# Performance work log

Measured on AMD Instinct MI355X. Metric: run time of the kernel, lower is better.

Reference implementation:

```python
import jax, jax.numpy as jnp
import numpy as np

HEADS = 8


def setup_inputs() -> dict:
    key = jax.random.key(0)
    k1, k2, k3, k4, k5 = jax.random.split(key, 5)
    bt, b_sz, n, dim = 2, 4, 1024, 512
    inner6 = 3072  # inner_dim * 6 where inner_dim = heads * dim_head = 512
    return {
        "x": jax.random.normal(k1, (bt, b_sz, n, dim), dtype=jnp.float32),
        "W_qkv": jax.random.normal(k2, (dim, inner6), dtype=jnp.float32) * 0.02,
        "b_qkv": jax.random.normal(k3, (inner6,), dtype=jnp.float32) * 0.02,
        "W_out": jax.random.normal(k4, (1024, dim), dtype=jnp.float32) * 0.02,
        "b_out": jax.random.normal(k5, (dim,), dtype=jnp.float32) * 0.02,
    }


def reference(x, W_qkv, b_qkv, W_out, b_out):
    bt, b_sz, n, dim = x.shape
    # to_qkv: Linear(dim, 3072) -> reshape (bt,b,n,3,H,hd) -> transpose(2,4)
    qkv = (x @ W_qkv + b_qkv).reshape(bt, b_sz, n, 3, HEADS, -1)
    qkv = qkv.transpose(0, 1, 4, 3, 2, 5)  # (bt, b, H, 3, n, hd)
    q, k, v = qkv[:, :, :, 0], qkv[:, :, :, 1], qkv[:, :, :, 2]
    scale = (dim // HEADS) ** -0.5  # faithful: uses dim//heads, not per-head width
    attn = jax.nn.softmax(jnp.einsum("abhnd,abhmd->abhnm", q * scale, k), axis=-1)
    out = jnp.einsum("abhnm,abhmd->abhnd", attn, v)
    out = out.transpose(0, 1, 3, 2, 4).reshape(bt, b_sz, n, -1)  # (bt,b,n,H*hd)
    return out @ W_out + b_out
```

## Files before the change

kernel.cpp:

```cpp
#include <hip/hip_runtime.h>

typedef __attribute__((ext_vector_type(4))) float f32x4;
typedef __attribute__((ext_vector_type(16))) float f32x16;
typedef __attribute__((ext_vector_type(8))) __bf16 bf16x8;
typedef __attribute__((ext_vector_type(8))) unsigned short ushortx8;
typedef __attribute__((ext_vector_type(4))) unsigned short ushortx4;
typedef unsigned short u16;
typedef unsigned int u32;

#define AS1 __attribute__((address_space(1)))
#define AS3 __attribute__((address_space(3)))

__device__ __forceinline__ void gld_lds16(const void* g, void* s) {
  __builtin_amdgcn_global_load_lds((AS1 void*)g, (AS3 void*)s, 16, 0, 0);
}

__device__ __forceinline__ u16 f2bf(float f) {
  unsigned int u = __float_as_uint(f);
  unsigned int r = (u + 0x7FFFu + ((u >> 16) & 1u)) >> 16;
  return (u16)r;
}

#define QSCALE 0.1803368801111244f

__global__ __launch_bounds__(256) void prep_fused(
    const float* __restrict__ x, u16* __restrict__ xb,
    const float* __restrict__ bqkv, float* __restrict__ bq2,
    const float* __restrict__ Wqkv, u16* __restrict__ wqkvt,
    const float* __restrict__ Wout, u16* __restrict__ woutt) {
  const int gid = blockIdx.x, tid = threadIdx.x;
  if (gid < 2048) {
    const int i = (gid * 256 + tid) * 8;
    const float4 a = *(const float4*)&x[i];
    const float4 b = *(const float4*)&x[i + 4];
    ushortx8 o;
    o[0] = f2bf(a.x); o[1] = f2bf(a.y); o[2] = f2bf(a.z); o[3] = f2bf(a.w);
    o[4] = f2bf(b.x); o[5] = f2bf(b.y); o[6] = f2bf(b.z); o[7] = f2bf(b.w);
    *(ushortx8*)&xb[i] = o;
    return;
  }
  __shared__ float tile[32][33];
  const int tx = tid & 31, ty = tid >> 5;
  if (gid < 3584) {
    const int t = gid - 2048;
    const int c0 = (t % 96) * 32, r0 = (t / 96) * 32;
    #pragma unroll
    for (int i = ty; i < 32; i += 8)
      tile[i][tx] = Wqkv[(size_t)(r0 + i) * 3072 + c0 + tx];
    __syncthreads();
    #pragma unroll
    for (int i = ty; i < 32; i += 8) {
      const float sc = (c0 + i < 1024) ? QSCALE : 1.0f;
      wqkvt[(size_t)(c0 + i) * 512 + r0 + tx] = f2bf(tile[tx][i] * sc);
    }
    return;
  }
  if (gid < 4096) {
    const int t = gid - 3584;
    const int c0 = (t % 16) * 32, r0 = (t / 16) * 32;
    #pragma unroll
    for (int i = ty; i < 32; i += 8)
      tile[i][tx] = Wout[(size_t)(r0 + i) * 512 + c0 + tx];
    __syncthreads();
    #pragma unroll
    for (int i = ty; i < 32; i += 8)
      woutt[(size_t)(c0 + i) * 1024 + r0 + tx] = f2bf(tile[tx][i]);
    return;
  }
  const int i = (gid - 4096) * 256 + tid;
  if (i < 3072) bq2[i] = bqkv[i] * (i < 1024 ? QSCALE : 1.0f);
}

template <int BM, int BN, int BK, int OUT_BF16>
__global__ __launch_bounds__(256, 4) void gemm_bt(const u16* __restrict__ A,
                                                  const u16* __restrict__ Bt,
                                                  const float* __restrict__ bias,
                                                  void* __restrict__ Cv,
                                                  int M, int N, int K) {
  constexpr int RPC = 512 / BK;
  constexpr int LPR = BK / 8;
  constexpr int MASK = LPR - 1;
  constexpr int P = 64 / BK > 0 ? 64 / BK : 1;
  constexpr int CA = BM / RPC, CB = BN / RPC;
  constexpr int CAW = CA / 4, CBW = CB / 4;
  constexpr int VM = CAW + CBW;
  constexpr int FM = BM / 32, FN = BN / 32;
  constexpr int KS = BK / 32;

  __shared__ __attribute__((aligned(16))) u16 As[2][BM * BK];
  __shared__ __attribute__((aligned(16))) u16 Bs[2][BN * BK];
  const int nwg = gridDim.x * gridDim.y;
  int bid = blockIdx.y * gridDim.x + blockIdx.x;
  if ((nwg & 7) == 0) bid = (bid & 7) * (nwg >> 3) + (bid >> 3);
  const int n0 = (bid % gridDim.x) * BN, m0 = (bid / gridDim.x) * BM;
  const int tid = threadIdx.x;
  const int w = tid >> 6, l = tid & 63;
  const int wr = w >> 1, wc = w & 1;
  const int lr = l >> 4, lc = l & 15;
  f32x4 acc[FM][FN] = {};

#define GSTAGE(bi, k0)                                                          \
  do {                                                                          \
    _Pragma("unroll") for (int i = 0; i < CAW; ++i) {                           \
      const int c = w * CAW + i;                                                \
      const int row = c * RPC + l / LPR;                                        \
      const int col = ((l % LPR) ^ ((row / P) & MASK)) * 8;                     \
      gld_lds16(&A[(size_t)(m0 + row) * K + (k0) + col], &As[bi][c * 512]);     \
    }                                                                           \
    _Pragma("unroll") for (int i = 0; i < CBW; ++i) {                           \
      const int c = w * CBW + i;                                                \
      const int row = c * RPC + l / LPR;                                        \
      const int col = ((l % LPR) ^ ((row / P) & MASK)) * 8;                     \
      gld_lds16(&Bt[(size_t)(n0 + row) * K + (k0) + col], &Bs[bi][c * 512]);    \
    }                                                                           \
  } while (0)

#define GCOMP(bi)                                                                      \
  do {                                                                                 \
    _Pragma("unroll") for (int ks = 0; ks < KS; ++ks) {                                \
      bf16x8 af[FM], bfr[FN];                                                          \
      _Pragma("unroll") for (int m = 0; m < FM; ++m) {                                 \
        const int row = wr * (BM / 2) + m * 16 + lc;                                   \
        af[m] = *(const bf16x8*)&As[bi][row * BK +                                     \
                                        (((ks * 4 + lr) ^ ((row / P) & MASK)) << 3)];  \
      }                                                                                \
      _Pragma("unroll") for (int n = 0; n < FN; ++n) {                                 \
        const int row = wc * (BN / 2) + n * 16 + lc;                                   \
        bfr[n] = *(const bf16x8*)&Bs[bi][row * BK +                                    \
                                         (((ks * 4 + lr) ^ ((row / P) & MASK)) << 3)]; \
      }                                                                                \
      __builtin_amdgcn_s_setprio(1);                                                   \
      _Pragma("unroll") for (int m = 0; m < FM; ++m)                                   \
          _Pragma("unroll") for (int n = 0; n < FN; ++n)                               \
              acc[m][n] =                                                              \
          __builtin_amdgcn_mfma_f32_16x16x32_bf16(af[m], bfr[n], acc[m][n], 0, 0, 0);  \
      __builtin_amdgcn_s_setprio(0);                                                   \
    }                                                                                  \
  } while (0)

  GSTAGE(0, 0);
  int buf = 0;
  for (int k0 = BK; k0 < K; k0 += BK) {
    GSTAGE(buf ^ 1, k0);
    if constexpr (VM == 2)
      asm volatile("s_waitcnt vmcnt(2)" ::: "memory");
    else if constexpr (VM == 3)
      asm volatile("s_waitcnt vmcnt(3)" ::: "memory");
    else if constexpr (VM == 4)
      asm volatile("s_waitcnt vmcnt(4)" ::: "memory");
    else
      asm volatile("s_waitcnt vmcnt(8)" ::: "memory");
    __builtin_amdgcn_s_barrier();
    __builtin_amdgcn_sched_barrier(0);
    GCOMP(buf);
    __builtin_amdgcn_s_barrier();
    buf ^= 1;
  }
  asm volatile("s_waitcnt vmcnt(0)" ::: "memory");
  __builtin_amdgcn_s_barrier();
  __builtin_amdgcn_sched_barrier(0);
  GCOMP(buf);
#undef GSTAGE
#undef GCOMP

  #pragma unroll
  for (int n = 0; n < FN; ++n) {
    const int col = n0 + wc * (BN / 2) + n * 16 + lc;
    const float bv = bias[col];
    #pragma unroll
    for (int m = 0; m < FM; ++m) {
      #pragma unroll
      for (int r = 0; r < 4; ++r) {
        const int row = m0 + wr * (BM / 2) + m * 16 + lr * 4 + r;
        const float v = acc[m][n][r] + bv;
        if (OUT_BF16)
          ((u16*)Cv)[(size_t)row * N + col] = f2bf(v);
        else
          ((float*)Cv)[(size_t)row * N + col] = v;
      }
    }
  }
}

__global__ __launch_bounds__(512, 2) void gemm_qkv_8ph(const u16* __restrict__ A,
                                                       const u16* __restrict__ Bt,
                                                       const float* __restrict__ bias,
                                                       u16* __restrict__ C,
                                                       u16* __restrict__ vt,
                                                       int M, int N, int K) {
  __shared__ __attribute__((aligned(16))) u16 SMEM[57344];
  u16* const AsP[2] = {SMEM, SMEM + 16384};
  u16* const BsP[2] = {SMEM + 32768, SMEM + 45056};
  const int nwg = gridDim.x;
  int bid = blockIdx.x;
  if ((nwg & 7) == 0) bid = (bid & 7) * (nwg >> 3) + (bid >> 3);
  const int ntile = N / 192;
  const int n0 = (bid % ntile) * 192, m0 = (bid / ntile) * 256;
  const int tid = threadIdx.x;
  const int w = tid >> 6, l = tid & 63;
  const int wr = w >> 2, wc = w & 3;
  const int lr = l >> 4, lc = l & 15;
  f32x4 acc[8][3] = {};
  bf16x8 af[2][2], bfv[3][2];

#define STAGE_A(bi, kt, h)                                                          \
  do {                                                                              \
    _Pragma("unroll") for (int cc = 0; cc < 2; ++cc) {                              \
      const int cib = (h) * 1024 + (cc * 8 + w) * 64;                               \
      const int ci = cib + l;                                                       \
      const int row = ci >> 3, ck = ci & 7;                                         \
      gld_lds16(&A[(size_t)(m0 + row) * K + (kt) * 64 + ((ck ^ (row & 7)) << 3)],   \
                &AsP[bi][cib * 8]);                                                 \
    }                                                                               \
  } while (0)

#define STAGE_B(bi, kt, t)                                                          \
  do {                                                                              \
    const int cib = (t) * 512 + w * 64;                                             \
    const int ci = cib + l;                                                         \
    const int row = ci >> 3, ck = ci & 7;                                           \
    gld_lds16(&Bt[(size_t)(n0 + row) * K + (kt) * 64 + ((ck ^ (row & 7)) << 3)],    \
              &BsP[bi][cib * 8]);                                                   \
  } while (0)

#define RD_A(bi, mp)                                                                \
  do {                                                                              \
    _Pragma("unroll") for (int m2 = 0; m2 < 2; ++m2)                                \
      _Pragma("unroll") for (int ks = 0; ks < 2; ++ks) {                            \
        const int row = wr * 128 + (2 * (mp) + m2) * 16 + lc;                       \
        af[m2][ks] = *(const bf16x8*)&AsP[bi][row * 64 +                            \
                                              (((ks * 4 + lr) ^ (lc & 7)) << 3)];   \
      }                                                                             \
  } while (0)

#define RD_B(bi)                                                                    \
  do {                                                                              \
    _Pragma("unroll") for (int n = 0; n < 3; ++n)                                   \
      _Pragma("unroll") for (int ks = 0; ks < 2; ++ks) {                            \
        const int row = wc * 48 + n * 16 + lc;                                      \
        bfv[n][ks] = *(const bf16x8*)&BsP[bi][row * 64 +                            \
                                              (((ks * 4 + lr) ^ (lc & 7)) << 3)];   \
      }                                                                             \
  } while (0)

#define MM(mp)                                                                      \
  do {                                                                              \
    __builtin_amdgcn_s_setprio(1);                                                  \
    _Pragma("unroll") for (int m2 = 0; m2 < 2; ++m2)                                \
      _Pragma("unroll") for (int n = 0; n < 3; ++n)                                 \
        _Pragma("unroll") for (int ks = 0; ks < 2; ++ks)                            \
          acc[2 * (mp) + m2][n] = __builtin_amdgcn_mfma_f32_16x16x32_bf16(          \
              af[m2][ks], bfv[n][ks], acc[2 * (mp) + m2][n], 0, 0, 0);              \
    __builtin_amdgcn_s_setprio(0);                                                  \
  } while (0)

#define BARC()                                                                      \
  do {                                                                              \
    __builtin_amdgcn_s_barrier();                                                   \
    asm volatile("s_waitcnt lgkmcnt(0)" ::: "memory");                              \
    __builtin_amdgcn_sched_barrier(0);                                              \
  } while (0)

  STAGE_B(0, 0, 0); STAGE_B(0, 0, 1); STAGE_B(0, 0, 2);
  STAGE_A(0, 0, 0); STAGE_A(0, 0, 1);
  STAGE_B(1, 1, 0); STAGE_B(1, 1, 1);
  asm volatile("s_waitcnt vmcnt(2)" ::: "memory");
  __builtin_amdgcn_s_barrier();
  __builtin_amdgcn_sched_barrier(0);

  const int NI = K >> 7;
  for (int i = 0; i < NI; ++i) {
    const bool nl = (i < NI - 1);
    const int tO = 2 * i + 1, tE2 = 2 * i + 2, tO2 = 2 * i + 3;
    RD_B(0); RD_A(0, 0);
    STAGE_B(1, tO, 2); STAGE_A(1, tO, 0); STAGE_A(1, tO, 1);
    BARC(); MM(0);
    __builtin_amdgcn_s_barrier();
    RD_A(0, 1);
    if (nl) STAGE_B(0, tE2, 0);
    BARC(); MM(1);
    __builtin_amdgcn_s_barrier();
    RD_A(0, 2);
    if (nl) STAGE_B(0, tE2, 1);
    BARC(); MM(2);
    __builtin_amdgcn_s_barrier();
    RD_A(0, 3);
    if (nl) STAGE_B(0, tE2, 2);
    BARC(); MM(3);
    if (nl) asm volatile("s_waitcnt vmcnt(3)" ::: "memory");
    else    asm volatile("s_waitcnt vmcnt(0)" ::: "memory");
    __builtin_amdgcn_s_barrier();
    __builtin_amdgcn_sched_barrier(0);
    RD_B(1); RD_A(1, 0);
    if (nl) STAGE_A(0, tE2, 0);
    BARC(); MM(0);
    __builtin_amdgcn_s_barrier();
    RD_A(1, 1);
    if (nl) STAGE_A(0, tE2, 1);
    BARC(); MM(1);
    __builtin_amdgcn_s_barrier();
    RD_A(1, 2);
    if (nl) STAGE_B(1, tO2, 0);
    BARC(); MM(2);
    __builtin_amdgcn_s_barrier();
    RD_A(1, 3);
    if (nl) STAGE_B(1, tO2, 1);
    BARC(); MM(3);
    if (nl) {
      asm volatile("s_waitcnt vmcnt(2)" ::: "memory");
      __builtin_amdgcn_s_barrier();
      __builtin_amdgcn_sched_barrier(0);
    }
  }
#undef STAGE_A
#undef STAGE_B
#undef RD_A
#undef RD_B
#undef MM
#undef BARC

  __builtin_amdgcn_s_barrier();
  const int b_idx = m0 >> 10;
  const int tok0 = m0 & 1023;
  #pragma unroll
  for (int n = 0; n < 3; ++n) {
    const int gc = n0 + wc * 48 + n * 16 + lc;
    const float bv = bias[gc];
    if (gc < 2048) {
      #pragma unroll
      for (int m = 0; m < 8; ++m)
        #pragma unroll
        for (int r = 0; r < 4; ++r) {
          const int row = wr * 128 + m * 16 + lr * 4 + r;
          SMEM[row * 192 + wc * 48 + n * 16 + lc] = f2bf(acc[m][n][r] + bv);
        }
    } else {
      const int hd = gc - 2048;
      u16* vrow = vt + ((size_t)(b_idx * 8 + (hd >> 7)) * 128 + (hd & 127)) * 1024;
      #pragma unroll
      for (int m = 0; m < 8; ++m) {
        const int tok = tok0 + wr * 128 + m * 16 + lr * 4;
        ushortx4 o;
        o[0] = f2bf(acc[m][n][0] + bv);
        o[1] = f2bf(acc[m][n][1] + bv);
        o[2] = f2bf(acc[m][n][2] + bv);
        o[3] = f2bf(acc[m][n][3] + bv);
        *(ushortx4*)&vrow[tok] = o;
      }
    }
  }
  __builtin_amdgcn_s_barrier();
  #pragma unroll
  for (int it = 0; it < 12; ++it) {
    const int chunk = it * 512 + tid;
    const int row = chunk / 24, c16 = chunk % 24;
    if (n0 + c16 * 8 < 2048) {
      const bf16x8 v = *(const bf16x8*)&SMEM[row * 192 + c16 * 8];
      *(bf16x8*)&C[(size_t)(m0 + row) * N + n0 + c16 * 8] = v;
    }
  }
}

__global__ __launch_bounds__(256, 2) void attn_fwd(const u16* __restrict__ qkv,
                                                   const u16* __restrict__ vt,
                                                   u16* __restrict__ attn_out) {
  __shared__ __attribute__((aligned(16))) u16 Ks[2][64 * 128];
  __shared__ __attribute__((aligned(16))) u16 Vs[2][64 * 128];
  const int orig = blockIdx.y * 8 + blockIdx.x;
  const int swz = (orig & 7) * 64 + (orig >> 3);
  const int bh = swz >> 3, b = bh >> 3, h = bh & 7;
  const int q0 = (swz & 7) * 128;
  const int tid = threadIdx.x, w = tid >> 6, l = tid & 63;
  const int ll = l & 31, hi = l >> 5;
  const int wq0 = q0 + w * 32;
  const u16* Qb = qkv + (size_t)(b * 1024 + wq0) * 3072 + h * 128;
  const u16* Kb = qkv + (size_t)(b * 1024) * 3072 + 1024 + h * 128;
  const u16* Vb = vt + (size_t)(b * 8 + h) * 128 * 1024;

  bf16x8 bq[8];
  #pragma unroll
  for (int s = 0; s < 8; ++s)
    bq[s] = *(const bf16x8*)&Qb[(size_t)ll * 3072 + s * 16 + hi * 8];
  asm volatile("s_waitcnt vmcnt(0)" ::: "memory");

  bf16x8 ones;
  #pragma unroll
  for (int i = 0; i < 8; ++i) ones[i] = (__bf16)1.0f;

  const u16* sb[8];
  int dst0;
  if (w < 2) {
    #pragma unroll
    for (int j = 0; j < 8; ++j) {
      const int r = w * 32 + j * 4 + (l >> 4);
      const int c = l & 15;
      sb[j] = Kb + (size_t)r * 3072 + ((c ^ (r & 15)) << 3);
    }
    dst0 = w * 4096;
  } else {
    #pragma unroll
    for (int j = 0; j < 8; ++j) {
      const int r2 = (w - 2) * 32 + j * 4 + (l >> 4);
      const int c = l & 15;
      const int d = ((c >> 3) ^ ((r2 >> 3) & 1)) * 64 + (r2 >> 5) * 32 + (r2 & 31);
      const int kc = (c & 7) ^ (r2 & 7);
      sb[j] = Vb + (size_t)d * 1024 + (kc << 3);
    }
    dst0 = (w - 2) * 4096;
  }

#define STAGE(bi, tt)                                                            \
  do {                                                                           \
    if (w < 2) {                                                                 \
      _Pragma("unroll") for (int j = 0; j < 8; ++j)                              \
          gld_lds16(sb[j] + (size_t)(tt)*196608, &Ks[bi][dst0 + j * 512]);       \
    } else {                                                                     \
      _Pragma("unroll") for (int j = 0; j < 8; ++j)                              \
          gld_lds16(sb[j] + (size_t)(tt)*64, &Vs[bi][dst0 + j * 512]);           \
    }                                                                            \
  } while (0)

#define QK(Kt)                                                                     \
  do {                                                                            \
    st0 = (f32x16){};                                                             \
    st1 = (f32x16){};                                                             \
    __builtin_amdgcn_s_setprio(1);                                                \
    _Pragma("unroll") for (int s = 0; s < 8; ++s) {                               \
      const int ch = ((s * 2 + hi) ^ (ll & 15)) << 3;                             \
      const bf16x8 ak0 = *(const bf16x8*)&(Kt)[ll * 128 + ch];                    \
      const bf16x8 ak1 = *(const bf16x8*)&(Kt)[(32 + ll) * 128 + ch];             \
      st0 = __builtin_amdgcn_mfma_f32_32x32x16_bf16(ak0, bq[s], st0, 0, 0, 0);    \
      st1 = __builtin_amdgcn_mfma_f32_32x32x16_bf16(ak1, bq[s], st1, 0, 0, 0);    \
    }                                                                             \
    __builtin_amdgcn_s_setprio(0);                                                \
  } while (0)

#define SOFTMAX()                                                                  \
  do {                                                                            \
    _Pragma("unroll") for (int kb = 0; kb < 2; ++kb) {                            \
      float pe[16];                                                               \
      _Pragma("unroll") for (int r = 0; r < 16; ++r)                              \
          pe[r] = exp2f(kb ? st1[r] : st0[r]);                                    \
      _Pragma("unroll") for (int j = 0; j < 8; ++j) {                             \
        u32 d_;                                                                   \
        asm("v_cvt_pk_bf16_f32 %0, %1, %2"                                        \
            : "=v"(d_)                                                            \
            : "v"(pe[2 * j]), "v"(pe[2 * j + 1]));                                \
        mm[kb * 8 + j] = d_;                                                      \
      }                                                                           \
      asm volatile("v_permlane32_swap_b32 %0, %1"                                 \
                   : "+v"(mm[kb * 8 + 0]), "+v"(mm[kb * 8 + 2]));                 \
      asm volatile("v_permlane32_swap_b32 %0, %1"                                 \
                   : "+v"(mm[kb * 8 + 1]), "+v"(mm[kb * 8 + 3]));                 \
      asm volatile("v_permlane32_swap_b32 %0, %1"                                 \
                   : "+v"(mm[kb * 8 + 4]), "+v"(mm[kb * 8 + 6]));                 \
      asm volatile("v_permlane32_swap_b32 %0, %1"                                 \
                   : "+v"(mm[kb * 8 + 5]), "+v"(mm[kb * 8 + 7]));                 \
    }                                                                             \
  } while (0)

#define PV(Vt_)                                                                    \
  do {                                                                            \
    __builtin_amdgcn_s_setprio(1);                                                \
    _Pragma("unroll") for (int kb = 0; kb < 2; ++kb) {                            \
      _Pragma("unroll") for (int s2 = 0; s2 < 2; ++s2) {                          \
        union { u32 u[4]; bf16x8 v; } pu;                                         \
        pu.u[0] = mm[kb * 8 + s2 * 4 + 0];                                        \
        pu.u[1] = mm[kb * 8 + s2 * 4 + 1];                                        \
        pu.u[2] = mm[kb * 8 + s2 * 4 + 2];                                        \
        pu.u[3] = mm[kb * 8 + s2 * 4 + 3];                                        \
        const bf16x8 pa = pu.v;                                                   \
        acc_l = __builtin_amdgcn_mfma_f32_32x32x16_bf16(pa, ones, acc_l, 0, 0, 0);\
        _Pragma("unroll") for (int db = 0; db < 4; ++db) {                        \
          const int r2 = (db & 1) * 32 + ll;                                      \
          const int c = ((((db >> 1) ^ ((ll >> 3) & 1)) << 3) |                   \
                         ((kb * 4 + s2 * 2 + hi) ^ (ll & 7)));                    \
          const bf16x8 bv = *(const bf16x8*)&(Vt_)[r2 * 128 + c * 8];             \
          acc_o[db] =                                                             \
              __builtin_amdgcn_mfma_f32_32x32x16_bf16(pa, bv, acc_o[db], 0, 0, 0);\
        }                                                                         \
      }                                                                           \
    }                                                                             \
    __builtin_amdgcn_s_setprio(0);                                                \
  } while (0)

  f32x16 acc_o[4] = {};
  f32x16 acc_l = {};
  f32x16 st0, st1;
  u32 mm[16];

  STAGE(0, 0);
  int buf = 0;
  for (int t = 0; t < 15; ++t) {
    STAGE(buf ^ 1, t + 1);
    asm volatile("s_waitcnt vmcnt(8)" ::: "memory");
    __builtin_amdgcn_s_barrier();
    __builtin_amdgcn_sched_barrier(0);
    QK(Ks[buf]);
    SOFTMAX();
    PV(Vs[buf]);
    __builtin_amdgcn_s_barrier();
    buf ^= 1;
  }
  asm volatile("s_waitcnt vmcnt(0)" ::: "memory");
  __builtin_amdgcn_s_barrier();
  __builtin_amdgcn_sched_barrier(0);
  QK(Ks[buf]);
  SOFTMAX();
  PV(Vs[buf]);

#undef STAGE
#undef QK
#undef SOFTMAX
#undef PV

  float inv[16];
  #pragma unroll
  for (int r = 0; r < 16; ++r) inv[r] = __builtin_amdgcn_rcpf(acc_l[r]);
  u16* Ob = attn_out + (size_t)(b * 1024 + wq0) * 1024 + h * 128;
  #pragma unroll
  for (int db = 0; db < 4; ++db)
    #pragma unroll
    for (int r = 0; r < 16; ++r) {
      const int q = (r & 3) + 8 * (r >> 2) + 4 * hi;
      Ob[(size_t)q * 1024 + db * 32 + ll] = f2bf(acc_o[db][r] * inv[r]);
    }
}

extern "C" void kernel_launch(void* const* d_in, const int* in_sizes, int n_in,
                              void* d_out, int out_size, void* d_ws, size_t ws_size,
                              hipStream_t stream) {
  const float* x = (const float*)d_in[0];
  const float* Wqkv = (const float*)d_in[1];
  const float* bqkv = (const float*)d_in[2];
  const float* Wout = (const float*)d_in[3];
  const float* bout = (const float*)d_in[4];
  float* out = (float*)d_out;

  char* ws = (char*)d_ws;
  u16* xb    = (u16*)(ws);
  u16* wqkvt = (u16*)(ws + 8388608);
  u16* woutt = (u16*)(ws + 8388608 + 3145728);
  u16* qkvb  = (u16*)(ws + 12582912);
  u16* vtb   = (u16*)(ws + 62914560);
  u16* aob   = (u16*)(ws + 79691776);
  float* bq2 = (float*)aob;

  prep_fused<<<4108, 256, 0, stream>>>(x, xb, bqkv, bq2, Wqkv, wqkvt, Wout, woutt);

  gemm_qkv_8ph<<<dim3(512), 512, 0, stream>>>(xb, wqkvt, bq2, qkvb, vtb,
                                              8192, 3072, 512);

  attn_fwd<<<dim3(8, 64), 256, 0, stream>>>(qkvb, vtb, aob);

  gemm_bt<128, 64, 32, 0><<<dim3(8, 64), 256, 0, stream>>>(aob, woutt, bout, out,
                                                           8192, 512, 1024);
}
```

Before: 116.7 us.

## Restructure double-buffer loops to use a single barrier per stage

Reworks the double-buffered pipelines in the GEMM, fused QKV GEMM and attention kernels so each iteration waits for all outstanding loads, issues one barrier, then issues the next stage's loads before computing. This drops the trailing barrier per iteration, and in the ping-pong GEMM it moves the LDS wait ahead of the barrier and merges adjacent barrier pairs. The cost is that the next tile's global loads are issued later, after the barrier, and the wait is now vmcnt(0), so less load latency may be hidden behind compute.

```diff
diff --git a/kernel.cpp b/kernel.cpp
--- a/kernel.cpp
+++ b/kernel.cpp
@@ -83,7 +83,6 @@
   constexpr int P = 64 / BK > 0 ? 64 / BK : 1;
   constexpr int CA = BM / RPC, CB = BN / RPC;
   constexpr int CAW = CA / 4, CBW = CB / 4;
-  constexpr int VM = CAW + CBW;
   constexpr int FM = BM / 32, FN = BN / 32;
   constexpr int KS = BK / 32;
 
@@ -140,26 +139,14 @@
 
   GSTAGE(0, 0);
   int buf = 0;
-  for (int k0 = BK; k0 < K; k0 += BK) {
-    GSTAGE(buf ^ 1, k0);
-    if constexpr (VM == 2)
-      asm volatile("s_waitcnt vmcnt(2)" ::: "memory");
-    else if constexpr (VM == 3)
-      asm volatile("s_waitcnt vmcnt(3)" ::: "memory");
-    else if constexpr (VM == 4)
-      asm volatile("s_waitcnt vmcnt(4)" ::: "memory");
-    else
-      asm volatile("s_waitcnt vmcnt(8)" ::: "memory");
+  for (int k0 = 0; k0 < K; k0 += BK) {
+    asm volatile("s_waitcnt vmcnt(0)" ::: "memory");
     __builtin_amdgcn_s_barrier();
     __builtin_amdgcn_sched_barrier(0);
+    if (k0 + BK < K) GSTAGE(buf ^ 1, k0 + BK);
     GCOMP(buf);
-    __builtin_amdgcn_s_barrier();
     buf ^= 1;
   }
-  asm volatile("s_waitcnt vmcnt(0)" ::: "memory");
-  __builtin_amdgcn_s_barrier();
-  __builtin_amdgcn_sched_barrier(0);
-  GCOMP(buf);
 #undef GSTAGE
 #undef GCOMP
 
@@ -254,10 +241,10 @@
     __builtin_amdgcn_s_setprio(0);                                                  \
   } while (0)
 
-#define BARC()                                                                      \
+#define SEAL()                                                                      \
   do {                                                                              \
+    asm volatile("s_waitcnt lgkmcnt(0)" ::: "memory");                              \
     __builtin_amdgcn_s_barrier();                                                   \
-    asm volatile("s_waitcnt lgkmcnt(0)" ::: "memory");                              \
     __builtin_amdgcn_sched_barrier(0);                                              \
   } while (0)
 
@@ -274,50 +261,44 @@
     const int tO = 2 * i + 1, tE2 = 2 * i + 2, tO2 = 2 * i + 3;
     RD_B(0); RD_A(0, 0);
     STAGE_B(1, tO, 2); STAGE_A(1, tO, 0); STAGE_A(1, tO, 1);
-    BARC(); MM(0);
-    __builtin_amdgcn_s_barrier();
+    SEAL(); MM(0);
     RD_A(0, 1);
     if (nl) STAGE_B(0, tE2, 0);
-    BARC(); MM(1);
-    __builtin_amdgcn_s_barrier();
+    SEAL(); MM(1);
     RD_A(0, 2);
     if (nl) STAGE_B(0, tE2, 1);
-    BARC(); MM(2);
-    __builtin_amdgcn_s_barrier();
+    SEAL(); MM(2);
     RD_A(0, 3);
     if (nl) STAGE_B(0, tE2, 2);
-    BARC(); MM(3);
+    asm volatile("s_waitcnt lgkmcnt(0)" ::: "memory");
     if (nl) asm volatile("s_waitcnt vmcnt(3)" ::: "memory");
     else    asm volatile("s_waitcnt vmcnt(0)" ::: "memory");
     __builtin_amdgcn_s_barrier();
     __builtin_amdgcn_sched_barrier(0);
+    MM(3);
     RD_B(1); RD_A(1, 0);
     if (nl) STAGE_A(0, tE2, 0);
-    BARC(); MM(0);
-    __builtin_amdgcn_s_barrier();
+    SEAL(); MM(0);
     RD_A(1, 1);
     if (nl) STAGE_A(0, tE2, 1);
-    BARC(); MM(1);
-    __builtin_amdgcn_s_barrier();
+    SEAL(); MM(1);
     RD_A(1, 2);
     if (nl) STAGE_B(1, tO2, 0);
-    BARC(); MM(2);
-    __builtin_amdgcn_s_barrier();
+    SEAL(); MM(2);
     RD_A(1, 3);
     if (nl) STAGE_B(1, tO2, 1);
-    BARC(); MM(3);
-    if (nl) {
-      asm volatile("s_waitcnt vmcnt(2)" ::: "memory");
-      __builtin_amdgcn_s_barrier();
-      __builtin_amdgcn_sched_barrier(0);
-    }
+    asm volatile("s_waitcnt lgkmcnt(0)" ::: "memory");
+    if (nl) asm volatile("s_waitcnt vmcnt(2)" ::: "memory");
+    __builtin_amdgcn_s_barrier();
+    __builtin_amdgcn_sched_barrier(0);
+    MM(3);
   }
 #undef STAGE_A
 #undef STAGE_B
 #undef RD_A
 #undef RD_B
 #undef MM
-#undef BARC
+#undef SEAL
 
   __builtin_amdgcn_s_barrier();
   const int b_idx = m0 >> 10;
@@ -491,23 +472,16 @@
 
   STAGE(0, 0);
   int buf = 0;
-  for (int t = 0; t < 15; ++t) {
-    STAGE(buf ^ 1, t + 1);
-    asm volatile("s_waitcnt vmcnt(8)" ::: "memory");
+  for (int t = 0; t < 16; ++t) {
+    asm volatile("s_waitcnt vmcnt(0)" ::: "memory");
     __builtin_amdgcn_s_barrier();
     __builtin_amdgcn_sched_barrier(0);
+    if (t < 15) STAGE(buf ^ 1, t + 1);
     QK(Ks[buf]);
     SOFTMAX();
     PV(Vs[buf]);
-    __builtin_amdgcn_s_barrier();
     buf ^= 1;
   }
-  asm volatile("s_waitcnt vmcnt(0)" ::: "memory");
-  __builtin_amdgcn_s_barrier();
-  __builtin_amdgcn_sched_barrier(0);
-  QK(Ks[buf]);
-  SOFTMAX();
-  PV(Vs[buf]);
 
 #undef STAGE
 #undef QK
```

Result: no change. 118.2 us (+1.3%).

## Shrink attention blocks to two waves and drop LDS double buffering

Applied to the files above, without the earlier changes.

The attention kernel now runs 128-thread blocks covering 64 queries each, launching twice as many blocks. K/V staging moves to a single LDS buffer (32KB instead of 64KB), loaded synchronously each tile with vmcnt(0), so more blocks can share a CU. The first QK MFMA uses a zero constant instead of explicit clears, and exp2f is replaced by the hardware exp2 builtin. The trade-off is losing load/compute overlap inside a block and doubling K/V global traffic per query, in the hope that the extra resident blocks hide the latency instead.

```diff
diff --git a/kernel.cpp b/kernel.cpp
--- a/kernel.cpp
+++ b/kernel.cpp
@@ -361,15 +361,15 @@
   }
 }
 
-__global__ __launch_bounds__(256, 2) void attn_fwd(const u16* __restrict__ qkv,
+__global__ __launch_bounds__(128, 4) void attn_fwd(const u16* __restrict__ qkv,
                                                    const u16* __restrict__ vt,
                                                    u16* __restrict__ attn_out) {
-  __shared__ __attribute__((aligned(16))) u16 Ks[2][64 * 128];
-  __shared__ __attribute__((aligned(16))) u16 Vs[2][64 * 128];
-  const int orig = blockIdx.y * 8 + blockIdx.x;
-  const int swz = (orig & 7) * 64 + (orig >> 3);
-  const int bh = swz >> 3, b = bh >> 3, h = bh & 7;
-  const int q0 = (swz & 7) * 128;
+  __shared__ __attribute__((aligned(16))) u16 Ks[64 * 128];
+  __shared__ __attribute__((aligned(16))) u16 Vs[64 * 128];
+  const int orig = blockIdx.y * 16 + blockIdx.x;
+  const int swz = (orig & 7) * 128 + (orig >> 3);
+  const int bh = swz >> 4, b = bh >> 3, h = bh & 7;
+  const int q0 = (swz & 15) * 64;
   const int tid = threadIdx.x, w = tid >> 6, l = tid & 63;
   const int ll = l & 31, hi = l >> 5;
   const int wq0 = q0 + w * 32;
@@ -386,49 +386,52 @@
   bf16x8 ones;
   #pragma unroll
   for (int i = 0; i < 8; ++i) ones[i] = (__bf16)1.0f;
-
-  const u16* sb[8];
-  int dst0;
-  if (w < 2) {
-    #pragma unroll
-    for (int j = 0; j < 8; ++j) {
-      const int r = w * 32 + j * 4 + (l >> 4);
+  const f32x16 fz = {};
+
+  const u16* sb[16];
+  if (w == 0) {
+    #pragma unroll
+    for (int j = 0; j < 16; ++j) {
+      const int r = j * 4 + (l >> 4);
       const int c = l & 15;
       sb[j] = Kb + (size_t)r * 3072 + ((c ^ (r & 15)) << 3);
     }
-    dst0 = w * 4096;
   } else {
     #pragma unroll
-    for (int j = 0; j < 8; ++j) {
-      const int r2 = (w - 2) * 32 + j * 4 + (l >> 4);
+    for (int j = 0; j < 16; ++j) {
+      const int r2 = j * 4 + (l >> 4);
       const int c = l & 15;
       const int d = ((c >> 3) ^ ((r2 >> 3) & 1)) * 64 + (r2 >> 5) * 32 + (r2 & 31);
       const int kc = (c & 7) ^ (r2 & 7);
       sb[j] = Vb + (size_t)d * 1024 + (kc << 3);
     }
-    dst0 = (w - 2) * 4096;
-  }
-
-#define STAGE(bi, tt)                                                            \
+  }
+
+#define STAGE(tt)                                                                \
   do {                                                                           \
-    if (w < 2) {                                                                 \
-      _Pragma("unroll") for (int j = 0; j < 8; ++j)                              \
-          gld_lds16(sb[j] + (size_t)(tt)*196608, &Ks[bi][dst0 + j * 512]);       \
+    if (w == 0) {                                                                \
+      _Pragma("unroll") for (int j = 0; j < 16; ++j)                             \
+          gld_lds16(sb[j] + (size_t)(tt)*196608, &Ks[j * 512]);                  \
     } else {                                                                     \
-      _Pragma("unroll") for (int j = 0; j < 8; ++j)                              \
-          gld_lds16(sb[j] + (size_t)(tt)*64, &Vs[bi][dst0 + j * 512]);           \
+      _Pragma("unroll") for (int j = 0; j < 16; ++j)                             \
+          gld_lds16(sb[j] + (size_t)(tt)*64, &Vs[j * 512]);                      \
     }                                                                            \
   } while (0)
 
-#define QK(Kt)                                                                     \
+#define QK()                                                                       \
   do {                                                                            \
-    st0 = (f32x16){};                                                             \
-    st1 = (f32x16){};                                                             \
     __builtin_amdgcn_s_setprio(1);                                                \
-    _Pragma("unroll") for (int s = 0; s < 8; ++s) {                               \
+    {                                                                             \
+      const int ch = (hi ^ (ll & 15)) << 3;                                       \
+      const bf16x8 a0 = *(const bf16x8*)&Ks[ll * 128 + ch];                       \
+      const bf16x8 a1 = *(const bf16x8*)&Ks[(32 + ll) * 128 + ch];                \
+      st0 = __builtin_amdgcn_mfma_f32_32x32x16_bf16(a0, bq[0], fz, 0, 0, 0);      \
+      st1 = __builtin_amdgcn_mfma_f32_32x32x16_bf16(a1, bq[0], fz, 0, 0, 0);      \
+    }                                                                             \
+    _Pragma("unroll") for (int s = 1; s < 8; ++s) {                               \
       const int ch = ((s * 2 + hi) ^ (ll & 15)) << 3;                             \
-      const bf16x8 ak0 = *(const bf16x8*)&(Kt)[ll * 128 + ch];                    \
-      const bf16x8 ak1 = *(const bf16x8*)&(Kt)[(32 + ll) * 128 + ch];             \
+      const bf16x8 ak0 = *(const bf16x8*)&Ks[ll * 128 + ch];                      \
+      const bf16x8 ak1 = *(const bf16x8*)&Ks[(32 + ll) * 128 + ch];               \
       st0 = __builtin_amdgcn_mfma_f32_32x32x16_bf16(ak0, bq[s], st0, 0, 0, 0);    \
       st1 = __builtin_amdgcn_mfma_f32_32x32x16_bf16(ak1, bq[s], st1, 0, 0, 0);    \
     }                                                                             \
@@ -440,7 +443,7 @@
     _Pragma("unroll") for (int kb = 0; kb < 2; ++kb) {                            \
       float pe[16];                                                               \
       _Pragma("unroll") for (int r = 0; r < 16; ++r)                              \
-          pe[r] = exp2f(kb ? st1[r] : st0[r]);                                    \
+          pe[r] = __builtin_amdgcn_exp2f(kb ? st1[r] : st0[r]);                   \
       _Pragma("unroll") for (int j = 0; j < 8; ++j) {                             \
         u32 d_;                                                                   \
         asm("v_cvt_pk_bf16_f32 %0, %1, %2"                                        \
@@ -459,7 +462,7 @@
     }                                                                             \
   } while (0)
 
-#define PV(Vt_)                                                                    \
+#define PV()                                                                       \
   do {                                                                            \
     __builtin_amdgcn_s_setprio(1);                                                \
     _Pragma("unroll") for (int kb = 0; kb < 2; ++kb) {                            \
@@ -475,7 +478,7 @@
           const int r2 = (db & 1) * 32 + ll;                                      \
           const int c = ((((db >> 1) ^ ((ll >> 3) & 1)) << 3) |                   \
                          ((kb * 4 + s2 * 2 + hi) ^ (ll & 7)));                    \
-          const bf16x8 bv = *(const bf16x8*)&(Vt_)[r2 * 128 + c * 8];             \
+          const bf16x8 bv = *(const bf16x8*)&Vs[r2 * 128 + c * 8];                \
           acc_o[db] =                                                             \
               __builtin_amdgcn_mfma_f32_32x32x16_bf16(pa, bv, acc_o[db], 0, 0, 0);\
         }                                                                         \
@@ -489,25 +492,16 @@
   f32x16 st0, st1;
   u32 mm[16];
 
-  STAGE(0, 0);
-  int buf = 0;
-  for (int t = 0; t < 15; ++t) {
-    STAGE(buf ^ 1, t + 1);
-    asm volatile("s_waitcnt vmcnt(8)" ::: "memory");
+  for (int t = 0; t < 16; ++t) {
+    STAGE(t);
+    asm volatile("s_waitcnt vmcnt(0)" ::: "memory");
     __builtin_amdgcn_s_barrier();
     __builtin_amdgcn_sched_barrier(0);
-    QK(Ks[buf]);
+    QK();
     SOFTMAX();
-    PV(Vs[buf]);
-    __builtin_amdgcn_s_barrier();
-    buf ^= 1;
-  }
-  asm volatile("s_waitcnt vmcnt(0)" ::: "memory");
-  __builtin_amdgcn_s_barrier();
-  __builtin_amdgcn_sched_barrier(0);
-  QK(Ks[buf]);
-  SOFTMAX();
-  PV(Vs[buf]);
+    PV();
+    if (t < 15) __builtin_amdgcn_s_barrier();
+  }
 
 #undef STAGE
 #undef QK
@@ -551,7 +545,7 @@
   gemm_qkv_8ph<<<dim3(512), 512, 0, stream>>>(xb, wqkvt, bq2, qkvb, vtb,
                                               8192, 3072, 512);
 
-  attn_fwd<<<dim3(8, 64), 256, 0, stream>>>(qkvb, vtb, aob);
+  attn_fwd<<<dim3(16, 64), 128, 0, stream>>>(qkvb, vtb, aob);
 
   gemm_bt<128, 64, 32, 0><<<dim3(8, 64), 256, 0, stream>>>(aob, woutt, bout, out,
                                                            8192, 512, 1024);
```

Result: slower. 133.3 us (+14.2%).

## Load K and V fragments directly from global memory in attention, dropping LDS staging

Applied to the files above, without the earlier changes.

Removes the double-buffered LDS pipeline (global_load_lds staging, barriers, swizzled LDS reads) from the attention kernel. Each wave now reads its K and V MFMA operands straight from global memory (relying on L1/L2) and runs the QK, exp and PV steps per tile with no block synchronisation. This saves LDS traffic and barriers, but each of the four waves now fetches the same K/V tiles separately, with non-contiguous access and no explicit prefetch, so memory latency may be exposed.

```diff
diff --git a/kernel.cpp b/kernel.cpp
--- a/kernel.cpp
+++ b/kernel.cpp
@@ -364,8 +364,6 @@
 __global__ __launch_bounds__(256, 2) void attn_fwd(const u16* __restrict__ qkv,
                                                    const u16* __restrict__ vt,
                                                    u16* __restrict__ attn_out) {
-  __shared__ __attribute__((aligned(16))) u16 Ks[2][64 * 128];
-  __shared__ __attribute__((aligned(16))) u16 Vs[2][64 * 128];
   const int orig = blockIdx.y * 8 + blockIdx.x;
   const int swz = (orig & 7) * 64 + (orig >> 3);
   const int bh = swz >> 3, b = bh >> 3, h = bh & 7;
@@ -381,138 +379,80 @@
   #pragma unroll
   for (int s = 0; s < 8; ++s)
     bq[s] = *(const bf16x8*)&Qb[(size_t)ll * 3072 + s * 16 + hi * 8];
-  asm volatile("s_waitcnt vmcnt(0)" ::: "memory");
 
   bf16x8 ones;
   #pragma unroll
   for (int i = 0; i < 8; ++i) ones[i] = (__bf16)1.0f;
-
-  const u16* sb[8];
-  int dst0;
-  if (w < 2) {
-    #pragma unroll
-    for (int j = 0; j < 8; ++j) {
-      const int r = w * 32 + j * 4 + (l >> 4);
-      const int c = l & 15;
-      sb[j] = Kb + (size_t)r * 3072 + ((c ^ (r & 15)) << 3);
-    }
-    dst0 = w * 4096;
-  } else {
-    #pragma unroll
-    for (int j = 0; j < 8; ++j) {
-      const int r2 = (w - 2) * 32 + j * 4 + (l >> 4);
-      const int c = l & 15;
-      const int d = ((c >> 3) ^ ((r2 >> 3) & 1)) * 64 + (r2 >> 5) * 32 + (r2 & 31);
-      const int kc = (c & 7) ^ (r2 & 7);
-      sb[j] = Vb + (size_t)d * 1024 + (kc << 3);
-    }
-    dst0 = (w - 2) * 4096;
-  }
-
-#define STAGE(bi, tt)                                                            \
-  do {                                                                           \
-    if (w < 2) {                                                                 \
-      _Pragma("unroll") for (int j = 0; j < 8; ++j)                              \
-          gld_lds16(sb[j] + (size_t)(tt)*196608, &Ks[bi][dst0 + j * 512]);       \
-    } else {                                                                     \
-      _Pragma("unroll") for (int j = 0; j < 8; ++j)                              \
-          gld_lds16(sb[j] + (size_t)(tt)*64, &Vs[bi][dst0 + j * 512]);           \
-    }                                                                            \
-  } while (0)
-
-#define QK(Kt)                                                                     \
-  do {                                                                            \
-    st0 = (f32x16){};                                                             \
-    st1 = (f32x16){};                                                             \
-    __builtin_amdgcn_s_setprio(1);                                                \
-    _Pragma("unroll") for (int s = 0; s < 8; ++s) {                               \
-      const int ch = ((s * 2 + hi) ^ (ll & 15)) << 3;                             \
-      const bf16x8 ak0 = *(const bf16x8*)&(Kt)[ll * 128 + ch];                    \
-      const bf16x8 ak1 = *(const bf16x8*)&(Kt)[(32 + ll) * 128 + ch];             \
-      st0 = __builtin_amdgcn_mfma_f32_32x32x16_bf16(ak0, bq[s], st0, 0, 0, 0);    \
-      st1 = __builtin_amdgcn_mfma_f32_32x32x16_bf16(ak1, bq[s], st1, 0, 0, 0);    \
-    }                                                                             \
-    __builtin_amdgcn_s_setprio(0);                                                \
-  } while (0)
-
-#define SOFTMAX()                                                                  \
-  do {                                                                            \
-    _Pragma("unroll") for (int kb = 0; kb < 2; ++kb) {                            \
-      float pe[16];                                                               \
-      _Pragma("unroll") for (int r = 0; r < 16; ++r)                              \
-          pe[r] = exp2f(kb ? st1[r] : st0[r]);                                    \
-      _Pragma("unroll") for (int j = 0; j < 8; ++j) {                             \
-        u32 d_;                                                                   \
-        asm("v_cvt_pk_bf16_f32 %0, %1, %2"                                        \
-            : "=v"(d_)                                                            \
-            : "v"(pe[2 * j]), "v"(pe[2 * j + 1]));                                \
-        mm[kb * 8 + j] = d_;                                                      \
-      }                                                                           \
-      asm volatile("v_permlane32_swap_b32 %0, %1"                                 \
-                   : "+v"(mm[kb * 8 + 0]), "+v"(mm[kb * 8 + 2]));                 \
-      asm volatile("v_permlane32_swap_b32 %0, %1"                                 \
-                   : "+v"(mm[kb * 8 + 1]), "+v"(mm[kb * 8 + 3]));                 \
-      asm volatile("v_permlane32_swap_b32 %0, %1"                                 \
-                   : "+v"(mm[kb * 8 + 4]), "+v"(mm[kb * 8 + 6]));                 \
-      asm volatile("v_permlane32_swap_b32 %0, %1"                                 \
-                   : "+v"(mm[kb * 8 + 5]), "+v"(mm[kb * 8 + 7]));                 \
-    }                                                                             \
-  } while (0)
-
-#define PV(Vt_)                                                                    \
-  do {                                                                            \
-    __builtin_amdgcn_s_setprio(1);                                                \
-    _Pragma("unroll") for (int kb = 0; kb < 2; ++kb) {                            \
-      _Pragma("unroll") for (int s2 = 0; s2 < 2; ++s2) {                          \
-        union { u32 u[4]; bf16x8 v; } pu;                                         \
-        pu.u[0] = mm[kb * 8 + s2 * 4 + 0];                                        \
-        pu.u[1] = mm[kb * 8 + s2 * 4 + 1];                                        \
-        pu.u[2] = mm[kb * 8 + s2 * 4 + 2];                                        \
-        pu.u[3] = mm[kb * 8 + s2 * 4 + 3];                                        \
-        const bf16x8 pa = pu.v;                                                   \
-        acc_l = __builtin_amdgcn_mfma_f32_32x32x16_bf16(pa, ones, acc_l, 0, 0, 0);\
-        _Pragma("unroll") for (int db = 0; db < 4; ++db) {                        \
-          const int r2 = (db & 1) * 32 + ll;                                      \
-          const int c = ((((db >> 1) ^ ((ll >> 3) & 1)) << 3) |                   \
-                         ((kb * 4 + s2 * 2 + hi) ^ (ll & 7)));                    \
-          const bf16x8 bv = *(const bf16x8*)&(Vt_)[r2 * 128 + c * 8];             \
-          acc_o[db] =                                                             \
-              __builtin_amdgcn_mfma_f32_32x32x16_bf16(pa, bv, acc_o[db], 0, 0, 0);\
-        }                                                                         \
-      }                                                                           \
-    }                                                                             \
-    __builtin_amdgcn_s_setprio(0);                                                \
-  } while (0)
+  const f32x16 fz = {};
+
+  const u16* kr0 = Kb + (size_t)ll * 3072 + hi * 8;
+  const u16* kr1 = Kb + (size_t)(ll + 32) * 3072 + hi * 8;
+  const u16* vr0 = Vb + (size_t)ll * 1024 + hi * 8;
 
   f32x16 acc_o[4] = {};
   f32x16 acc_l = {};
   f32x16 st0, st1;
   u32 mm[16];
 
-  STAGE(0, 0);
-  int buf = 0;
-  for (int t = 0; t < 15; ++t) {
-    STAGE(buf ^ 1, t + 1);
-    asm volatile("s_waitcnt vmcnt(8)" ::: "memory");
-    __builtin_amdgcn_s_barrier();
-    __builtin_amdgcn_sched_barrier(0);
-    QK(Ks[buf]);
-    SOFTMAX();
-    PV(Vs[buf]);
-    __builtin_amdgcn_s_barrier();
-    buf ^= 1;
-  }
-  asm volatile("s_waitcnt vmcnt(0)" ::: "memory");
-  __builtin_amdgcn_s_barrier();
-  __builtin_amdgcn_sched_barrier(0);
-  QK(Ks[buf]);
-  SOFTMAX();
-  PV(Vs[buf]);
-
-#undef STAGE
-#undef QK
-#undef SOFTMAX
-#undef PV
+  for (int t = 0; t < 16; ++t) {
+    const size_t kofs = (size_t)t * 196608;
+    {
+      const bf16x8 a0 = *(const bf16x8*)&kr0[kofs];
+      const bf16x8 a1 = *(const bf16x8*)&kr1[kofs];
+      st0 = __builtin_amdgcn_mfma_f32_32x32x16_bf16(a0, bq[0], fz, 0, 0, 0);
+      st1 = __builtin_amdgcn_mfma_f32_32x32x16_bf16(a1, bq[0], fz, 0, 0, 0);
+    }
+    #pragma unroll
+    for (int s = 1; s < 8; ++s) {
+      const bf16x8 ak0 = *(const bf16x8*)&kr0[kofs + s * 16];
+      const bf16x8 ak1 = *(const bf16x8*)&kr1[kofs + s * 16];
+      st0 = __builtin_amdgcn_mfma_f32_32x32x16_bf16(ak0, bq[s], st0, 0, 0, 0);
+      st1 = __builtin_amdgcn_mfma_f32_32x32x16_bf16(ak1, bq[s], st1, 0, 0, 0);
+    }
+    #pragma unroll
+    for (int kb = 0; kb < 2; ++kb) {
+      float pe[16];
+      #pragma unroll
+      for (int r = 0; r < 16; ++r)
+        pe[r] = __builtin_amdgcn_exp2f(kb ? st1[r] : st0[r]);
+      #pragma unroll
+      for (int j = 0; j < 8; ++j) {
+        u32 d_;
+        asm("v_cvt_pk_bf16_f32 %0, %1, %2"
+            : "=v"(d_)
+            : "v"(pe[2 * j]), "v"(pe[2 * j + 1]));
+        mm[kb * 8 + j] = d_;
+      }
+      asm volatile("v_permlane32_swap_b32 %0, %1"
+                   : "+v"(mm[kb * 8 + 0]), "+v"(mm[kb * 8 + 2]));
+      asm volatile("v_permlane32_swap_b32 %0, %1"
+                   : "+v"(mm[kb * 8 + 1]), "+v"(mm[kb * 8 + 3]));
+      asm volatile("v_permlane32_swap_b32 %0, %1"
+                   : "+v"(mm[kb * 8 + 4]), "+v"(mm[kb * 8 + 6]));
+      asm volatile("v_permlane32_swap_b32 %0, %1"
+                   : "+v"(mm[kb * 8 + 5]), "+v"(mm[kb * 8 + 7]));
+    }
+    #pragma unroll
+    for (int kb = 0; kb < 2; ++kb) {
+      #pragma unroll
+      for (int s2 = 0; s2 < 2; ++s2) {
+        union { u32 u[4]; bf16x8 v; } pu;
+        pu.u[0] = mm[kb * 8 + s2 * 4 + 0];
+        pu.u[1] = mm[kb * 8 + s2 * 4 + 1];
+        pu.u[2] = mm[kb * 8 + s2 * 4 + 2];
+        pu.u[3] = mm[kb * 8 + s2 * 4 + 3];
+        const bf16x8 pa = pu.v;
+        acc_l = __builtin_amdgcn_mfma_f32_32x32x16_bf16(pa, ones, acc_l, 0, 0, 0);
+        #pragma unroll
+        for (int db = 0; db < 4; ++db) {
+          const bf16x8 bv = *(const bf16x8*)&vr0[(size_t)db * 32768 + t * 64 +
+                                                 (kb * 4 + s2 * 2) * 8];
+          acc_o[db] =
+              __builtin_amdgcn_mfma_f32_32x32x16_bf16(pa, bv, acc_o[db], 0, 0, 0);
+        }
+      }
+    }
+  }
 
   float inv[16];
   #pragma unroll
```

After: 201.8 us. +72.8%, slower.
